# Performance work log

Measured on AMD Instinct MI355X. Metric: run time of the kernel, lower is better.

The kernel has to match this reference:

```python
import jax, jax.numpy as jnp
import numpy as np

M, N, D_MODEL = 16, 2048, 512
H, D = 8, 64  # num_heads, head_dim; inner_dim = H*D = 512


def setup_inputs() -> dict:
    key = jax.random.key(0)
    ks = jax.random.split(key, 8)
    s = 1.0 / np.sqrt(D_MODEL)
    return {
        "xq": jax.random.normal(ks[0], (M, N, D_MODEL), jnp.float32),
        "xk": jax.random.normal(ks[1], (M, N, D_MODEL), jnp.float32),
        "xv": jax.random.normal(ks[2], (M, N, D_MODEL), jnp.float32),
        "Wq": jax.random.normal(ks[3], (D_MODEL, H * D), jnp.float32) * s,
        "Wk": jax.random.normal(ks[4], (D_MODEL, H * D), jnp.float32) * s,
        "Wv": jax.random.normal(ks[5], (D_MODEL, H * D), jnp.float32) * s,
        "Wo": jax.random.normal(ks[6], (H * D, D_MODEL), jnp.float32) * s,
        "bo": jnp.zeros((D_MODEL,), jnp.float32),
    }


def _split_heads(x):
    # [m, n, h*d] -> [m, h, n, d]
    m, n, _ = x.shape
    return x.reshape(m, n, H, D).transpose(0, 2, 1, 3)


def reference(xq, xk, xv, Wq, Wk, Wv, Wo, bo):
    scale = D ** -0.5
    q = _split_heads(xq @ Wq)
    k = _split_heads(xk @ Wk)
    v = _split_heads(xv @ Wv)
    # linear attention: softmax over feature dim for both q and k
    q = jax.nn.softmax(q, axis=-1) * scale
    k = jax.nn.softmax(k, axis=-1)
    kv = jnp.einsum('mhnd,mhne->mhde', k, v)   # [m, h, d, d]
    out = jnp.einsum('mhqd,mhde->mhqe', q, kv)  # [m, h, nq, d]
    out = out.transpose(0, 2, 1, 3).reshape(out.shape[0], -1, H * D)
    return out @ Wo + bo
```

## Files before the change

kernel.cpp:

```cpp
#include <hip/hip_runtime.h>
#include <hip/hip_bf16.h>


typedef __bf16 bf16;
typedef __bf16 bf16x8 __attribute__((ext_vector_type(8)));
typedef __bf16 bf16x4 __attribute__((ext_vector_type(4)));
typedef float  f32x4  __attribute__((ext_vector_type(4)));

#define MFMA16(a, b, c) __builtin_amdgcn_mfma_f32_16x16x32_bf16((a), (b), (c), 0, 0, 0)

__device__ inline bf16x8 cvt8(float4 a, float4 b) {
  bf16x8 h;
  h[0] = (bf16)a.x; h[1] = (bf16)a.y; h[2] = (bf16)a.z; h[3] = (bf16)a.w;
  h[4] = (bf16)b.x; h[5] = (bf16)b.y; h[6] = (bf16)b.z; h[7] = (bf16)b.w;
  return h;
}

__device__ inline void glds16(const void* g, void* l) {
  __builtin_amdgcn_global_load_lds((const __attribute__((address_space(1))) void*)g,
                                   (__attribute__((address_space(3))) void*)l, 16, 0, 0);
}

__global__ __launch_bounds__(256) void k_prep(const float* __restrict__ w0, const float* __restrict__ w1,
                                              const float* __restrict__ w2, const float* __restrict__ w3,
                                              bf16* __restrict__ t0, bf16* __restrict__ t1,
                                              bf16* __restrict__ t2, bf16* __restrict__ t3)
{
  const float* W = (blockIdx.z == 0) ? w0 : (blockIdx.z == 1) ? w1 : (blockIdx.z == 2) ? w2 : w3;
  bf16*        T = (blockIdx.z == 0) ? t0 : (blockIdx.z == 1) ? t1 : (blockIdx.z == 2) ? t2 : t3;
  __shared__ float lds[64][68];
  const int t = threadIdx.x;
  const int r = t >> 2, c0 = (t & 3) << 4;
  const float* src = W + (size_t)(blockIdx.x * 64 + r) * 512 + blockIdx.y * 64 + c0;
  float4 f0 = ((const float4*)src)[0];
  float4 f1 = ((const float4*)src)[1];
  float4 f2 = ((const float4*)src)[2];
  float4 f3 = ((const float4*)src)[3];
  *(float4*)&lds[r][c0 + 0]  = f0;
  *(float4*)&lds[r][c0 + 4]  = f1;
  *(float4*)&lds[r][c0 + 8]  = f2;
  *(float4*)&lds[r][c0 + 12] = f3;
  __syncthreads();
  bf16 v[16];
#pragma unroll
  for (int s = 0; s < 16; ++s) v[s] = (bf16)lds[c0 + s][r];
  bf16* dst = T + (size_t)(blockIdx.y * 64 + r) * 512 + blockIdx.x * 64 + c0;
  *(bf16x8*)&dst[0] = *(bf16x8*)&v[0];
  *(bf16x8*)&dst[8] = *(bf16x8*)&v[8];
}

__global__ __launch_bounds__(512) void k_qkv(const float* __restrict__ xq, const float* __restrict__ xk,
                                             const float* __restrict__ xv,
                                             const bf16* __restrict__ WqT, const bf16* __restrict__ WkT,
                                             const bf16* __restrict__ WvT,
                                             bf16* __restrict__ Qo, bf16* __restrict__ Ko,
                                             bf16* __restrict__ Vo)
{
  const int wg = blockIdx.x;
  const int o  = (wg & 7) * 192 + (wg >> 3);
  const int proj = o >> 9;
  const int rem  = o & 511;
  const int rb = rem >> 1, cb = rem & 1;

  const float* X  = (proj == 0) ? xq  : (proj == 1) ? xk  : xv;
  const bf16*  WT = (proj == 0) ? WqT : (proj == 1) ? WkT : WvT;
  bf16*       OUT = (proj == 0) ? Qo  : (proj == 1) ? Ko  : Vo;

  __shared__ bf16 As[128][40];
  __shared__ bf16 Bs[256 * 32];

  const int t = threadIdx.x;
  const int lane = t & 63, w = t >> 6;
  const int wr = w >> 2, wc = w & 3;
  const int g = lane >> 4, li = lane & 15;
  const size_t arow = (size_t)rb * 128;

  const int ar = t >> 2, ac = (t & 3) << 3;
  const float* xp = X + (arow + ar) * 512 + ac;

  const bf16* bsrc = WT + (size_t)(cb * 256 + w * 32 + (lane >> 2)) * 512
                        + (((lane & 3) ^ ((lane >> 3) & 3)) << 3);
  char* bdst = (char*)&Bs[0] + w * 2048;
  const int bslot = g ^ ((li >> 1) & 3);

  f32x4 acc[4][4] = {};
  float4 xa0 = ((const float4*)xp)[0];
  float4 xa1 = ((const float4*)xp)[1];

  for (int kt = 0; kt < 16; ++kt) {
    __syncthreads();
    *(bf16x8*)&As[ar][ac] = cvt8(xa0, xa1);
#pragma unroll
    for (int j = 0; j < 2; ++j)
      glds16(bsrc + (size_t)j * 16 * 512 + kt * 32, bdst + j * 1024);
    __syncthreads();
    if (kt < 15) {
      xa0 = ((const float4*)(xp + (kt + 1) * 32))[0];
      xa1 = ((const float4*)(xp + (kt + 1) * 32))[1];
    }
    bf16x8 af[4], bfr[4];
#pragma unroll
    for (int rt = 0; rt < 4; ++rt)
      af[rt] = *(const bf16x8*)&As[wr * 64 + rt * 16 + li][g * 8];
#pragma unroll
    for (int ct = 0; ct < 4; ++ct)
      bfr[ct] = *(const bf16x8*)&Bs[(wc * 64 + ct * 16 + li) * 32 + bslot * 8];
#pragma unroll
    for (int rt = 0; rt < 4; ++rt)
#pragma unroll
      for (int ct = 0; ct < 4; ++ct)
        acc[rt][ct] = MFMA16(af[rt], bfr[ct], acc[rt][ct]);
  }

#pragma unroll
  for (int rt = 0; rt < 4; ++rt) {
#pragma unroll
    for (int q = 0; q < 4; ++q) {
      float v0 = acc[rt][0][q], v1 = acc[rt][1][q], v2 = acc[rt][2][q], v3 = acc[rt][3][q];
      if (proj < 2) {
        float mx = fmaxf(fmaxf(v0, v1), fmaxf(v2, v3));
        mx = fmaxf(mx, __shfl_xor(mx, 1));
        mx = fmaxf(mx, __shfl_xor(mx, 2));
        mx = fmaxf(mx, __shfl_xor(mx, 4));
        mx = fmaxf(mx, __shfl_xor(mx, 8));
        v0 = __expf(v0 - mx); v1 = __expf(v1 - mx); v2 = __expf(v2 - mx); v3 = __expf(v3 - mx);
        float s = v0 + v1 + v2 + v3;
        s += __shfl_xor(s, 1); s += __shfl_xor(s, 2); s += __shfl_xor(s, 4); s += __shfl_xor(s, 8);
        const float inv = (proj == 0 ? 0.125f : 1.0f) / s;
        v0 *= inv; v1 *= inv; v2 *= inv; v3 *= inv;
      }
      bf16* op = OUT + (arow + wr * 64 + rt * 16 + g * 4 + q) * 512 + cb * 256 + wc * 64 + li;
      op[0] = (bf16)v0; op[16] = (bf16)v1; op[32] = (bf16)v2; op[48] = (bf16)v3;
    }
  }
}

__global__ __launch_bounds__(256) void k_kv(const bf16* __restrict__ K, const bf16* __restrict__ V,
                                            float* __restrict__ kvp)
{
  const int mh = blockIdx.x, m = mh >> 3, h = mh & 7;
  const int ns = blockIdx.y;
  __shared__ bf16 Kt[64][40];
  __shared__ bf16 Vt[64][40];
  const int t = threadIdx.x, lane = t & 63, wave = t >> 6;
  const int dq = wave >> 1, eq = wave & 1;
  const int g = lane >> 4, li = lane & 15;
  const int tn = t & 31, d0 = (t >> 5) << 3;
  const size_t rowbase = (size_t)m * 2048 + ns * 512;

  f32x4 acc[2][2] = {};

  for (int nt = 0; nt < 16; ++nt) {
    __syncthreads();
    {
      bf16x8 kr = *(const bf16x8*)(K + (rowbase + nt * 32 + tn) * 512 + h * 64 + d0);
      bf16x8 vr = *(const bf16x8*)(V + (rowbase + nt * 32 + tn) * 512 + h * 64 + d0);
#pragma unroll
      for (int j = 0; j < 8; ++j) Kt[d0 + j][tn] = kr[j];
#pragma unroll
      for (int j = 0; j < 8; ++j) Vt[d0 + j][tn] = vr[j];
    }
    __syncthreads();
    bf16x8 af[2], bfr[2];
#pragma unroll
    for (int dt = 0; dt < 2; ++dt) af[dt]  = *(const bf16x8*)&Kt[dq * 32 + dt * 16 + li][g * 8];
#pragma unroll
    for (int et = 0; et < 2; ++et) bfr[et] = *(const bf16x8*)&Vt[eq * 32 + et * 16 + li][g * 8];
#pragma unroll
    for (int dt = 0; dt < 2; ++dt)
#pragma unroll
      for (int et = 0; et < 2; ++et)
        acc[dt][et] = MFMA16(af[dt], bfr[et], acc[dt][et]);
  }

  float* o = kvp + ((size_t)mh * 4 + ns) * 4096;
#pragma unroll
  for (int dt = 0; dt < 2; ++dt)
#pragma unroll
    for (int et = 0; et < 2; ++et)
#pragma unroll
      for (int q = 0; q < 4; ++q) {
        const int d = dq * 32 + dt * 16 + g * 4 + q;
        const int e = eq * 32 + et * 16 + li;
        o[d * 64 + e] = acc[dt][et][q];
      }
}

__global__ __launch_bounds__(512) void k_wfused(const float* __restrict__ kvp, const bf16* __restrict__ WoT,
                                                bf16* __restrict__ WfT)
{
  const int mh = blockIdx.x, m = mh >> 3, h = mh & 7;
  __shared__ bf16 kvs[64][72];
  const int t = threadIdx.x, lane = t & 63, wave = t >> 6;
  const int g = lane >> 4, li = lane & 15;
  {
    const int d = t >> 3, e0 = (t & 7) << 3;
    const float* p = kvp + (size_t)mh * 16384 + d * 64 + e0;
#pragma unroll
    for (int j = 0; j < 8; ++j) {
      float s = p[j] + p[4096 + j] + p[8192 + j] + p[12288 + j];
      kvs[d][e0 + j] = (bf16)s;
    }
  }
  __syncthreads();
  f32x4 acc[4][4] = {};
#pragma unroll
  for (int kk = 0; kk < 2; ++kk) {
    bf16x8 af[4], bfr[4];
#pragma unroll
    for (int rt = 0; rt < 4; ++rt) {
      const int c = wave * 64 + rt * 16 + li;
      af[rt] = *(const bf16x8*)(WoT + (size_t)c * 512 + h * 64 + kk * 32 + g * 8);
    }
#pragma unroll
    for (int ct = 0; ct < 4; ++ct)
      bfr[ct] = *(const bf16x8*)&kvs[ct * 16 + li][kk * 32 + g * 8];
#pragma unroll
    for (int rt = 0; rt < 4; ++rt)
#pragma unroll
      for (int ct = 0; ct < 4; ++ct)
        acc[rt][ct] = MFMA16(af[rt], bfr[ct], acc[rt][ct]);
  }
  bf16* o = WfT + (size_t)m * 262144;
#pragma unroll
  for (int rt = 0; rt < 4; ++rt)
#pragma unroll
    for (int ct = 0; ct < 4; ++ct)
#pragma unroll
      for (int q = 0; q < 4; ++q) {
        const int c = wave * 64 + rt * 16 + g * 4 + q;
        const int r = h * 64 + ct * 16 + li;
        o[(size_t)c * 512 + r] = (bf16)acc[rt][ct][q];
      }
}

__global__ __launch_bounds__(512) void k_out(const bf16* __restrict__ Q, const bf16* __restrict__ WfT,
                                             const float* __restrict__ bo, float* __restrict__ out)
{
  const int wg = blockIdx.x;
  const int o  = (wg & 7) * 64 + (wg >> 3);
  const int rb = o >> 1, cb = o & 1;
  const int m  = rb >> 4;
  const bf16* Bm = WfT + (size_t)m * 262144;

  __shared__ bf16 As2[128 * 32];
  __shared__ bf16 Bs2[256 * 32];

  const int t = threadIdx.x, lane = t & 63, w = t >> 6;
  const int wr = w >> 2, wc = w & 3;
  const int g = lane >> 4, li = lane & 15;
  const size_t arow = (size_t)rb * 128;

  const int schunk = ((lane & 3) ^ ((lane >> 3) & 3)) << 3;
  const bf16* asrc = Q + (arow + w * 16 + (lane >> 2)) * 512 + schunk;
  const bf16* bsrc = Bm + (size_t)(cb * 256 + w * 32 + (lane >> 2)) * 512 + schunk;
  char* adst = (char*)&As2[0] + w * 1024;
  char* bdst = (char*)&Bs2[0] + w * 2048;
  const int slot = g ^ ((li >> 1) & 3);

  f32x4 acc[4][4] = {};

  for (int kt = 0; kt < 16; ++kt) {
    __syncthreads();
    glds16(asrc + kt * 32, adst);
#pragma unroll
    for (int j = 0; j < 2; ++j)
      glds16(bsrc + (size_t)j * 16 * 512 + kt * 32, bdst + j * 1024);
    __syncthreads();
    bf16x8 af[4], bfr[4];
#pragma unroll
    for (int rt = 0; rt < 4; ++rt)
      af[rt] = *(const bf16x8*)&As2[(wr * 64 + rt * 16 + li) * 32 + slot * 8];
#pragma unroll
    for (int ct = 0; ct < 4; ++ct)
      bfr[ct] = *(const bf16x8*)&Bs2[(wc * 64 + ct * 16 + li) * 32 + slot * 8];
#pragma unroll
    for (int rt = 0; rt < 4; ++rt)
#pragma unroll
      for (int ct = 0; ct < 4; ++ct)
        acc[rt][ct] = MFMA16(af[rt], bfr[ct], acc[rt][ct]);
  }

  float bv[4];
#pragma unroll
  for (int ct = 0; ct < 4; ++ct) bv[ct] = bo[cb * 256 + wc * 64 + ct * 16 + li];
#pragma unroll
  for (int rt = 0; rt < 4; ++rt)
#pragma unroll
    for (int q = 0; q < 4; ++q) {
      float* op = out + (arow + wr * 64 + rt * 16 + g * 4 + q) * 512 + cb * 256 + wc * 64 + li;
      op[0]  = acc[rt][0][q] + bv[0];
      op[16] = acc[rt][1][q] + bv[1];
      op[32] = acc[rt][2][q] + bv[2];
      op[48] = acc[rt][3][q] + bv[3];
    }
}

extern "C" void kernel_launch(void* const* d_in, const int* in_sizes, int n_in,
                              void* d_out, int out_size, void* d_ws, size_t ws_size,
                              hipStream_t stream)
{
  const float* xq = (const float*)d_in[0];
  const float* xk = (const float*)d_in[1];
  const float* xv = (const float*)d_in[2];
  const float* Wq = (const float*)d_in[3];
  const float* Wk = (const float*)d_in[4];
  const float* Wv = (const float*)d_in[5];
  const float* Wo = (const float*)d_in[6];
  const float* bo = (const float*)d_in[7];
  float* out = (float*)d_out;

  char* ws = (char*)d_ws;
  const size_t WT_BYTES  = 512 * 512 * 2;
  const size_t QKV_BYTES = (size_t)32768 * 512 * 2;
  bf16*  WqT = (bf16*)(ws);
  bf16*  WkT = (bf16*)(ws + WT_BYTES);
  bf16*  WvT = (bf16*)(ws + 2 * WT_BYTES);
  bf16*  WoT = (bf16*)(ws + 3 * WT_BYTES);
  bf16*  Qb  = (bf16*)(ws + 4 * WT_BYTES);
  bf16*  Kb  = (bf16*)(ws + 4 * WT_BYTES + QKV_BYTES);
  bf16*  Vb  = (bf16*)(ws + 4 * WT_BYTES + 2 * QKV_BYTES);
  float* kvp = (float*)(ws + 4 * WT_BYTES + 3 * QKV_BYTES);
  bf16*  WfT = Kb;

  k_prep  <<<dim3(8, 8, 4), 256, 0, stream>>>(Wq, Wk, Wv, Wo, WqT, WkT, WvT, WoT);
  k_qkv   <<<dim3(1536),    512, 0, stream>>>(xq, xk, xv, WqT, WkT, WvT, Qb, Kb, Vb);
  k_kv    <<<dim3(128, 4),  256, 0, stream>>>(Kb, Vb, kvp);
  k_wfused<<<dim3(128),     512, 0, stream>>>(kvp, WoT, WfT);
  k_out   <<<dim3(512),     512, 0, stream>>>(Qb, WfT, bo, out);
}
```

Baseline: 164.5 us.

## Double-buffer LDS tiles in QKV and output GEMM kernels

```diff
diff --git a/kernel.cpp b/kernel.cpp
--- a/kernel.cpp
+++ b/kernel.cpp
@@ -66,8 +66,8 @@
   const bf16*  WT = (proj == 0) ? WqT : (proj == 1) ? WkT : WvT;
   bf16*       OUT = (proj == 0) ? Qo  : (proj == 1) ? Ko  : Vo;
 
-  __shared__ bf16 As[128][40];
-  __shared__ bf16 Bs[256 * 32];
+  __shared__ bf16 As[2][128][40];
+  __shared__ bf16 Bs[2][256 * 32];
 
   const int t = threadIdx.x;
   const int lane = t & 63, w = t >> 6;
@@ -80,36 +80,47 @@
 
   const bf16* bsrc = WT + (size_t)(cb * 256 + w * 32 + (lane >> 2)) * 512
                         + (((lane & 3) ^ ((lane >> 3) & 3)) << 3);
-  char* bdst = (char*)&Bs[0] + w * 2048;
   const int bslot = g ^ ((li >> 1) & 3);
 
   f32x4 acc[4][4] = {};
+
   float4 xa0 = ((const float4*)xp)[0];
   float4 xa1 = ((const float4*)xp)[1];
-
+  *(bf16x8*)&As[0][ar][ac] = cvt8(xa0, xa1);
+  xa0 = ((const float4*)(xp + 32))[0];
+  xa1 = ((const float4*)(xp + 32))[1];
+#pragma unroll
+  for (int j = 0; j < 2; ++j)
+    glds16(bsrc + (size_t)j * 16 * 512, (char*)&Bs[0][0] + w * 2048 + j * 1024);
+  __syncthreads();
+
+#pragma unroll
   for (int kt = 0; kt < 16; ++kt) {
-    __syncthreads();
-    *(bf16x8*)&As[ar][ac] = cvt8(xa0, xa1);
-#pragma unroll
-    for (int j = 0; j < 2; ++j)
-      glds16(bsrc + (size_t)j * 16 * 512 + kt * 32, bdst + j * 1024);
-    __syncthreads();
+    const int cur = kt & 1;
     if (kt < 15) {
-      xa0 = ((const float4*)(xp + (kt + 1) * 32))[0];
-      xa1 = ((const float4*)(xp + (kt + 1) * 32))[1];
+#pragma unroll
+      for (int j = 0; j < 2; ++j)
+        glds16(bsrc + (size_t)j * 16 * 512 + (kt + 1) * 32,
+               (char*)&Bs[cur ^ 1][0] + w * 2048 + j * 1024);
+      *(bf16x8*)&As[cur ^ 1][ar][ac] = cvt8(xa0, xa1);
+    }
+    if (kt < 14) {
+      xa0 = ((const float4*)(xp + (kt + 2) * 32))[0];
+      xa1 = ((const float4*)(xp + (kt + 2) * 32))[1];
     }
     bf16x8 af[4], bfr[4];
 #pragma unroll
     for (int rt = 0; rt < 4; ++rt)
-      af[rt] = *(const bf16x8*)&As[wr * 64 + rt * 16 + li][g * 8];
+      af[rt] = *(const bf16x8*)&As[cur][wr * 64 + rt * 16 + li][g * 8];
 #pragma unroll
     for (int ct = 0; ct < 4; ++ct)
-      bfr[ct] = *(const bf16x8*)&Bs[(wc * 64 + ct * 16 + li) * 32 + bslot * 8];
+      bfr[ct] = *(const bf16x8*)&Bs[cur][(wc * 64 + ct * 16 + li) * 32 + bslot * 8];
 #pragma unroll
     for (int rt = 0; rt < 4; ++rt)
 #pragma unroll
       for (int ct = 0; ct < 4; ++ct)
         acc[rt][ct] = MFMA16(af[rt], bfr[ct], acc[rt][ct]);
+    if (kt < 15) __syncthreads();
   }
 
 #pragma unroll
@@ -243,8 +254,8 @@
   const int m  = rb >> 4;
   const bf16* Bm = WfT + (size_t)m * 262144;
 
-  __shared__ bf16 As2[128 * 32];
-  __shared__ bf16 Bs2[256 * 32];
+  __shared__ bf16 As2[2][128 * 32];
+  __shared__ bf16 Bs2[2][256 * 32];
 
   const int t = threadIdx.x, lane = t & 63, w = t >> 6;
   const int wr = w >> 2, wc = w & 3;
@@ -254,31 +265,39 @@
   const int schunk = ((lane & 3) ^ ((lane >> 3) & 3)) << 3;
   const bf16* asrc = Q + (arow + w * 16 + (lane >> 2)) * 512 + schunk;
   const bf16* bsrc = Bm + (size_t)(cb * 256 + w * 32 + (lane >> 2)) * 512 + schunk;
-  char* adst = (char*)&As2[0] + w * 1024;
-  char* bdst = (char*)&Bs2[0] + w * 2048;
   const int slot = g ^ ((li >> 1) & 3);
 
   f32x4 acc[4][4] = {};
 
+  glds16(asrc, (char*)&As2[0][0] + w * 1024);
+#pragma unroll
+  for (int j = 0; j < 2; ++j)
+    glds16(bsrc + (size_t)j * 16 * 512, (char*)&Bs2[0][0] + w * 2048 + j * 1024);
+  __syncthreads();
+
+#pragma unroll
   for (int kt = 0; kt < 16; ++kt) {
-    __syncthreads();
-    glds16(asrc + kt * 32, adst);
-#pragma unroll
-    for (int j = 0; j < 2; ++j)
-      glds16(bsrc + (size_t)j * 16 * 512 + kt * 32, bdst + j * 1024);
-    __syncthreads();
+    const int cur = kt & 1;
+    if (kt < 15) {
+      glds16(asrc + (kt + 1) * 32, (char*)&As2[cur ^ 1][0] + w * 1024);
+#pragma unroll
+      for (int j = 0; j < 2; ++j)
+        glds16(bsrc + (size_t)j * 16 * 512 + (kt + 1) * 32,
+               (char*)&Bs2[cur ^ 1][0] + w * 2048 + j * 1024);
+    }
     bf16x8 af[4], bfr[4];
 #pragma unroll
     for (int rt = 0; rt < 4; ++rt)
-      af[rt] = *(const bf16x8*)&As2[(wr * 64 + rt * 16 + li) * 32 + slot * 8];
+      af[rt] = *(const bf16x8*)&As2[cur][(wr * 64 + rt * 16 + li) * 32 + slot * 8];
 #pragma unroll
     for (int ct = 0; ct < 4; ++ct)
-      bfr[ct] = *(const bf16x8*)&Bs2[(wc * 64 + ct * 16 + li) * 32 + slot * 8];
+      bfr[ct] = *(const bf16x8*)&Bs2[cur][(wc * 64 + ct * 16 + li) * 32 + slot * 8];
 #pragma unroll
     for (int rt = 0; rt < 4; ++rt)
 #pragma unroll
       for (int ct = 0; ct < 4; ++ct)
         acc[rt][ct] = MFMA16(af[rt], bfr[ct], acc[rt][ct]);
+    if (kt < 15) __syncthreads();
   }
 
   float bv[4];
```

New measurement: 167.9 us. 1.02x slower.
